# Performance work log

Measured on AMD Instinct MI355X. Metric: run time of the kernel, lower is better.

## Reference

```python
import jax, jax.numpy as jnp
import numpy as np

B, C, L, D, P, Q = 8, 32, 512, 128, 96, 3
LEVELS = 3
ORDERS = [1, 2, 3, 4]  # begin_order=1 + band index

# db4 decomposition low-pass filter (pywt convention)
_LO = np.array([-0.010597401784997278, 0.032883011666982945,
                0.030841381835986965, -0.18703481171888114,
                -0.02798376941698385, 0.6308807679295904,
                0.7148465705525415, 0.23037781330885523], dtype=np.float32)
FLEN = int(_LO.size)
_HI = (_LO[::-1] * ((-1.0) ** (np.arange(FLEN) + 1))).astype(np.float32)

DEC_LO_R = jnp.asarray(_LO[::-1].copy())  # correlation kernel = reversed dec_lo
DEC_HI_R = jnp.asarray(_HI[::-1].copy())
REC_LO_R = jnp.asarray(_LO.copy())        # rec_lo[::-1] == dec_lo (orthogonal wavelet)
REC_HI_R = jnp.asarray(_HI.copy())        # rec_hi[::-1] == dec_hi


def _corr(x, k, stride=1, pad=0):
    # batched 1D correlation; x: [N, Lx], k: [flen]
    return jax.lax.conv_general_dilated(
        x[:, None, :], k[None, None, :], (stride,), [(pad, pad)],
        dimension_numbers=('NCH', 'OIH', 'NCH'))[:, 0, :]


def dwt_step(x):
    # pywt.dwt, mode='symmetric': half-sample symmetric extension by flen-1,
    # correlate with reversed filter, sample odd positions. out len = (n+flen-1)//2
    p = FLEN - 1
    ext = jnp.concatenate([x[:, :p][:, ::-1], x, x[:, -p:][:, ::-1]], axis=1)
    e = ext[:, 1:]
    return _corr(e, DEC_LO_R, stride=2), _corr(e, DEC_HI_R, stride=2)


def idwt_step(a, d):
    # pywt.idwt: upsample-by-2, full convolution with rec filters, trim flen-2 per side
    n = a.shape[1]
    z = jnp.zeros((a.shape[0], 2 * n - 1), a.dtype)
    ua = z.at[:, ::2].set(a)
    ud = z.at[:, ::2].set(d)
    y = _corr(ua, REC_LO_R, pad=FLEN - 1) + _corr(ud, REC_HI_R, pad=FLEN - 1)
    t = FLEN - 2
    return y[:, t:y.shape[1] - t]


def dwt_bands(x):
    # x: [N, L] -> LEVELS+1 single-band reconstructions (wavedec + selective waverec)
    n = x.shape[1]
    a, dets = x, []
    for _ in range(LEVELS):
        a, d = dwt_step(a)
        dets.append(d)
    clist = [a] + dets[::-1]  # [cA_L, cD_L, ..., cD_1]
    bands = []
    for i in range(len(clist)):
        keep = [c if j == i else jnp.zeros_like(c) for j, c in enumerate(clist)]
        r = keep[0]
        for d in keep[1:]:
            if r.shape[1] == d.shape[1] + 1:  # pywt waverec length fixup
                r = r[:, :-1]
            r = idwt_step(r, d)
        bands.append(r[:, :n])
    return bands


def embed(x1, w):
    # TokenEmbedding: Conv1d(1, D, k=3, padding=1, circular, bias=False); x_mark=None
    xp = jnp.concatenate([x1[:, -1:], x1, x1[:, :1]], axis=1)[:, None, :]
    y = jax.lax.conv_general_dilated(xp, w, (1,), [(0, 0)],
                                     dimension_numbers=('NCH', 'OIH', 'NCH'))
    return y.transpose(0, 2, 1)  # [N, L, D]


def cheby(x, coeffs):
    # ChebyKANLinear: tanh squash, Chebyshev T_0..T_K-1 recurrence, contract with coeffs
    # x: [M, Din], coeffs: [Din, Dout, K]
    x = jnp.tanh(x)
    K = coeffs.shape[2]
    t_prev = jnp.ones_like(x)
    out = t_prev @ coeffs[:, :, 0]
    if K > 1:
        t = x
        out = out + t @ coeffs[:, :, 1]
        for k in range(2, K):
            t, t_prev = 2.0 * x * t - t_prev, t
            out = out + t @ coeffs[:, :, k]
    return out


def conv_same(x, w, b, dil):
    # x: [N, Ch, L]; Conv1d(C, C, 3, padding=dil, dilation=dil)
    y = jax.lax.conv_general_dilated(x, w, (1,), [(dil, dil)], rhs_dilation=(dil,),
                                     dimension_numbers=('NCH', 'OIH', 'NCH'))
    return y + b[None, :, None]


def tcn(x, w1, b1, w2, b2, dil):
    h = x.transpose(0, 2, 1)
    h = jax.nn.gelu(conv_same(h, w1, b1, dil), approximate=False)
    h = jax.nn.gelu(conv_same(h, w2, b2, dil), approximate=False)
    return h.transpose(0, 2, 1) + x  # residual (dropout is eval-mode identity)


def _forward(x_enc, emb_w, chebs, tcns, proj_w, proj_b, pred_w, pred_b):
    bsz = x_enc.shape[0]
    # use_norm=0 -> Normalize is identity; original detaches before CPU DWT
    x = jax.lax.stop_gradient(x_enc)
    xc = x.transpose(0, 2, 1).reshape(bsz * C, L)  # per-channel series
    bands = dwt_bands(xc)
    fused = jnp.zeros((bsz * C, L, D), x_enc.dtype)
    for i, band in enumerate(bands):
        emb = embed(band, emb_w)  # [B*C, L, D]
        x1 = cheby(emb.reshape(-1, D), chebs[i]).reshape(bsz * C, L, D)
        dil = max(1, 2 ** max(ORDERS[i] - 1, 0))
        fused = fused + x1 + tcn(emb, *tcns[i], dil)
    # predict_layer over time, projection over features
    h = jnp.einsum('nld,pl->npd', fused, pred_w) + pred_b[None, :, None]  # [B*C, P, D]
    out = jnp.einsum('npd,qd->npq', h, proj_w) + proj_b                  # [B*C, P, Q]
    return out.reshape(bsz, C, P, Q)[:, 0]  # channel 0, denorm is identity


def setup_inputs() -> dict:
    key = jax.random.key(0)
    ks = iter(jax.random.split(key, 64))
    inp = {'x_enc': jax.random.normal(next(ks), (B, L, C), jnp.float32)}
    inp['emb_w'] = jax.random.normal(next(ks), (D, 1, 3), jnp.float32) * (2.0 / 3.0) ** 0.5
    std = (2.0 / (D * 3)) ** 0.5
    for i, o in enumerate(ORDERS):
        K = o + 1
        inp[f'cheb{i}'] = jax.random.normal(next(ks), (D, D, K), jnp.float32) * (1.0 / (D * K))
        inp[f'tw1_{i}'] = jax.random.normal(next(ks), (D, D, 3), jnp.float32) * std
        inp[f'tb1_{i}'] = jnp.zeros((D,), jnp.float32)
        inp[f'tw2_{i}'] = jax.random.normal(next(ks), (D, D, 3), jnp.float32) * std
        inp[f'tb2_{i}'] = jnp.zeros((D,), jnp.float32)
    inp['proj_w'] = jax.random.normal(next(ks), (Q, D), jnp.float32) * D ** -0.5
    inp['proj_b'] = jnp.zeros((Q,), jnp.float32)
    inp['pred_w'] = jax.random.normal(next(ks), (P, L), jnp.float32) * L ** -0.5
    inp['pred_b'] = jnp.zeros((P,), jnp.float32)
    return inp


def reference(x_enc, emb_w, cheb0, tw1_0, tb1_0, tw2_0, tb2_0,
              cheb1, tw1_1, tb1_1, tw2_1, tb2_1,
              cheb2, tw1_2, tb1_2, tw2_2, tb2_2,
              cheb3, tw1_3, tb1_3, tw2_3, tb2_3,
              proj_w, proj_b, pred_w, pred_b):
    chebs = [cheb0, cheb1, cheb2, cheb3]
    tcns = [(tw1_0, tb1_0, tw2_0, tb2_0), (tw1_1, tb1_1, tw2_1, tb2_1),
            (tw1_2, tb1_2, tw2_2, tb2_2), (tw1_3, tb1_3, tw2_3, tb2_3)]
    return _forward(x_enc, emb_w, chebs, tcns, proj_w, proj_b, pred_w, pred_b)
```

## Files before the change

kernel.cpp:

```cpp
#include <hip/hip_runtime.h>
#include <math.h>

#define NB 8
#define LL 512
#define DD 128
#define PP 96
#define QQ 3

#define WS_BANDS 0
#define WS_CFR   16384
#define WS_WFR   (WS_CFR + 81920)
#define WS_B0    (WS_WFR + 196608)

typedef __attribute__((ext_vector_type(8))) short short8v;
typedef __attribute__((ext_vector_type(4))) float f32x4;

#define MFMA16(a, b, c) __builtin_amdgcn_mfma_f32_16x16x32_bf16(a, b, c, 0, 0, 0)

__device__ __forceinline__ short f2bf(float f) {
  unsigned u = __builtin_bit_cast(unsigned, f);
  unsigned r = (u + 0x7fffu + ((u >> 16) & 1u)) >> 16;
  return (short)r;
}

__device__ __forceinline__ float fast_tanh(float x) {
  float ax = fabsf(x);
  float e = __expf(-2.0f * ax);
  float r = (1.0f - e) / (1.0f + e);
  return x < 0.0f ? -r : r;
}

__device__ __forceinline__ float fast_gelu(float x) {
  float u = 0.7978845608028654f * x * (1.0f + 0.044715f * x * x);
  return 0.5f * x * (1.0f + fast_tanh(u));
}

constexpr float W_LO[8] = {
  -0.010597401784997278f, 0.032883011666982945f, 0.030841381835986965f,
  -0.18703481171888114f, -0.02798376941698385f, 0.6308807679295904f,
  0.7148465705525415f, 0.23037781330885523f
};

__device__ void dwt_level(const float* xin, int n, float* a, float* d,
                          int tid, int nthr) {
  int outn = (n + 5) / 2 + 1;
  for (int j = tid; j < outn; j += nthr) {
    float sa = 0.f, sd = 0.f;
#pragma unroll
    for (int k = 0; k < 8; ++k) {
      int i = 2 * j + k;
      int idx = (i < 6) ? (5 - i) : ((i < n + 6) ? (i - 6) : (2 * n + 5 - i));
      float v = xin[idx];
      sa += v * W_LO[7 - k];
      sd += v * ((k & 1) ? -W_LO[k] : W_LO[k]);
    }
    a[j] = sa;
    d[j] = sd;
  }
}

__device__ void idwt_level(const float* a, const float* d, float* out, int n,
                           int tid, int nthr) {
  int outn = 2 * n - 6;
  for (int t = tid; t < outn; t += nthr) {
    float s = 0.f;
#pragma unroll
    for (int k = 0; k < 8; ++k) {
      int j = t - 1 + k;
      if (j >= 0 && j <= 2 * n - 2 && ((j & 1) == 0)) {
        int m = j >> 1;
        if (a) s += a[m] * W_LO[k];
        if (d) s += d[m] * ((k & 1) ? W_LO[7 - k] : -W_LO[7 - k]);
      }
    }
    out[t] = s;
  }
}

struct PrepArgs {
  const float* x_enc;
  const float* cheb[4];
  const float* w1[4];
  const float* w2[4];
  const float* pred_b;
  const float* proj_w;
  const float* proj_b;
  float* bands;
  short* cfr;
  short* wfr;
  float* b0;
  float* out;
};

__global__ __launch_bounds__(256) void prep_kernel(PrepArgs a) {
  __shared__ float sx[LL];
  __shared__ float a1[259], d1[259], a2[133], d2[133], a3[70], d3[70];
  __shared__ float rA[LL], rB[LL];
  int bid = blockIdx.x, t = threadIdx.x;
  if (bid < 32) {
    int n = bid & 7, band = bid >> 3;
    for (int l = t; l < LL; l += 256)
      sx[l] = a.x_enc[(size_t)n * LL * 32 + (size_t)l * 32];
    __syncthreads();
    dwt_level(sx, 512, a1, d1, t, 256); __syncthreads();
    dwt_level(a1, 259, a2, d2, t, 256); __syncthreads();
    dwt_level(a2, 133, a3, d3, t, 256); __syncthreads();
    idwt_level(band == 0 ? a3 : nullptr, band == 1 ? d3 : nullptr, rA, 70, t, 256);
    __syncthreads();
    idwt_level(rA, band == 2 ? d2 : nullptr, rB, 133, t, 256);
    __syncthreads();
    idwt_level(rB, band == 3 ? d1 : nullptr, rA, 259, t, 256);
    __syncthreads();
    float* dstb = a.bands + ((size_t)band * NB + n) * LL;
    for (int l = t; l < LL; l += 256) dstb[l] = rA[l];
  } else {
    const int CFRG = 20480, WFRG = 49152, B0N = 512, OUTN = NB * PP * QQ;
    const int total = CFRG + WFRG + B0N + OUTN;
    for (int g = (bid - 32) * 256 + t; g < total; g += 128 * 256) {
      if (g < CFRG) {
        int s = g >> 11, r = g & 2047;
        int ks = r >> 9, r2 = r & 511;
        int nt = r2 >> 6, lane = r2 & 63;
        int b = (s >= 6) ? 3 : ((s >= 3) ? 2 : ((s >= 1) ? 1 : 0));
        int off = (b == 3) ? 6 : ((b == 2) ? 3 : ((b == 1) ? 1 : 0));
        int kl = s - off;
        int K = b + 2;
        int din0 = ks * 32 + (lane >> 4) * 8;
        int dout = nt * 16 + (lane & 15);
        const float* src = a.cheb[b];
        short8v v;
#pragma unroll
        for (int el = 0; el < 8; ++el)
          v[el] = f2bf(src[((size_t)(din0 + el) * DD + dout) * K + kl + 1]);
        ((short8v*)a.cfr)[g] = v;
      } else if (g < CFRG + WFRG) {
        int g2 = g - CFRG;
        int m = g2 >> 11, r = g2 & 2047;
        int ks = r >> 9, r2 = r & 511;
        int nt = r2 >> 6, lane = r2 & 63;
        int bw = m / 3, tap = m - bw * 3;
        int band = bw >> 1, which = bw & 1;
        const float* w = which ? a.w2[band] : a.w1[band];
        int din0 = ks * 32 + (lane >> 4) * 8;
        int dout = nt * 16 + (lane & 15);
        short8v v;
#pragma unroll
        for (int el = 0; el < 8; ++el)
          v[el] = f2bf(w[((size_t)dout * DD + din0 + el) * 3 + tap]);
        ((short8v*)a.wfr)[g2] = v;
      } else if (g < CFRG + WFRG + B0N) {
        int e4 = g - CFRG - WFRG;
        int b = e4 >> 7, dout = e4 & 127;
        int K = b + 2;
        const float* cw = a.cheb[b];
        float s2 = 0.f;
        for (int din = 0; din < DD; ++din) s2 += cw[((size_t)din * DD + dout) * K];
        a.b0[e4] = s2;
      } else {
        int e5 = g - CFRG - WFRG - B0N;
        int pq = e5 % (PP * QQ);
        int p = pq / QQ, q = pq - p * QQ;
        float S = 0.f;
        const float* pw = a.proj_w + (size_t)q * DD;
        for (int d = 0; d < DD; ++d) S += pw[d];
        a.out[e5] = a.pred_b[p] * S + a.proj_b[q];
      }
    }
  }
}

struct MainArgs {
  const float* emb_w;
  const float* bands;
  const short* cfr;
  const short* wfr;
  const float* proj_w;
  const float* pred_w;
  const float* b1[4];
  const float* b2[4];
  const float* b0;
  float* out;
};

__device__ __forceinline__ void proj_epilogue(
    const MainArgs& ar, int n, int l0, float* tile, float* red, float* gq) {
  int t = threadIdx.x;
  __syncthreads();
  if (t < 192) {
    int pair = t % 96, half = t / 96;
    int p_loc = pair / 3, q = pair - (pair / 3) * 3;
    const float* pw = ar.proj_w + (size_t)q * DD + half * 64;
    const float* tr = tile + p_loc * 132 + half * 64;
    float sv = 0.f;
#pragma unroll 8
    for (int d = 0; d < 64; ++d) sv += tr[d] * pw[d];
    red[t] = sv;
  }
  __syncthreads();
  if (t < 96) gq[t] = red[t] + red[96 + t];
  __syncthreads();
  if (t < PP) {
    const float* pw = ar.pred_w + (size_t)t * LL + l0;
    float s0 = 0.f, s1 = 0.f, s2 = 0.f;
#pragma unroll 8
    for (int l = 0; l < 32; ++l) {
      float w = pw[l];
      s0 += w * gq[l * 3 + 0];
      s1 += w * gq[l * 3 + 1];
      s2 += w * gq[l * 3 + 2];
    }
    float* op = ar.out + (size_t)n * (PP * QQ) + t * 3;
    atomicAdd(op + 0, s0);
    atomicAdd(op + 1, s1);
    atomicAdd(op + 2, s2);
  }
}

template <int NK>
__device__ __forceinline__ void cheby_core(
    const MainArgs& ar, int band, int n, int l0, short* sU, float* blx,
    float* red, float* gq) {
  int t = threadIdx.x;
  const float* brow = ar.bands + ((size_t)band * NB + n) * LL;
  const float* ew = ar.emb_w;
  if (t < 34) blx[t] = brow[(l0 - 1 + t + LL) & 511];
  __syncthreads();
  for (int idx = t; idx < 32 * DD; idx += 256) {
    int l = idx >> 7, dch = idx & 127;
    float e = ew[dch * 3] * blx[l] + ew[dch * 3 + 1] * blx[l + 1] +
              ew[dch * 3 + 2] * blx[l + 2];
    float x = fast_tanh(e);
    int o = l * 136 + dch;
    sU[o] = f2bf(x);
    if (NK >= 2) {
      float t2 = 2.f * x * x - 1.f;
      sU[4352 + o] = f2bf(t2);
      if (NK >= 3) {
        float t3 = 2.f * x * t2 - x;
        sU[8704 + o] = f2bf(t3);
        if (NK >= 4) sU[13056 + o] = f2bf(2.f * x * t3 - t2);
      }
    }
  }
  __syncthreads();

  int w = t >> 6, lane = t & 63;
  int r16 = lane & 15, kq = lane >> 4;
  const int sbase = NK * (NK - 1) / 2;
  const short8v* cfrv = (const short8v*)ar.cfr;
  f32x4 cacc[2][2];
#pragma unroll
  for (int i = 0; i < 2; ++i)
#pragma unroll
    for (int j = 0; j < 2; ++j) cacc[i][j] = (f32x4){0.f, 0.f, 0.f, 0.f};
#pragma unroll
  for (int s = 0; s < NK; ++s) {
#pragma unroll
    for (int ks = 0; ks < 4; ++ks) {
      short8v a0 = *(const short8v*)&sU[s * 4352 + r16 * 136 + ks * 32 + kq * 8];
      short8v a1 = *(const short8v*)&sU[s * 4352 + (16 + r16) * 136 + ks * 32 + kq * 8];
      short8v bf0 = cfrv[(((sbase + s) * 4 + ks) * 8 + w * 2 + 0) * 64 + lane];
      short8v bf1 = cfrv[(((sbase + s) * 4 + ks) * 8 + w * 2 + 1) * 64 + lane];
      cacc[0][0] = MFMA16(a0, bf0, cacc[0][0]);
      cacc[0][1] = MFMA16(a0, bf1, cacc[0][1]);
      cacc[1][0] = MFMA16(a1, bf0, cacc[1][0]);
      cacc[1][1] = MFMA16(a1, bf1, cacc[1][1]);
    }
  }
  __syncthreads();
  float* tile = (float*)sU;
  int row0 = kq * 4;
#pragma unroll
  for (int nt = 0; nt < 2; ++nt) {
    int dout = w * 32 + nt * 16 + r16;
    float b0v = ar.b0[band * DD + dout];
#pragma unroll
    for (int m = 0; m < 2; ++m)
#pragma unroll
      for (int r = 0; r < 4; ++r)
        tile[(m * 16 + row0 + r) * 132 + dout] = cacc[m][nt][r] + b0v;
  }
  proj_epilogue(ar, n, l0, tile, red, gq);
}

template <int DIL>
__device__ __forceinline__ void conv_core(
    const MainArgs& ar, int band, int n, int l0, short* sU, float* blx2,
    float* red, float* gq) {
  int t = threadIdx.x;
  const float* brow = ar.bands + ((size_t)band * NB + n) * LL;
  const float* ew = ar.emb_w;
  if (t < 66) blx2[t] = brow[(l0 - 2 * DIL - 1 + t + LL) & 511];
  __syncthreads();

  const int ETR = 32 + 4 * DIL;
  for (int idx = t; idx < ETR * DD; idx += 256) {
    int v = idx >> 7, dch = idx & 127;
    int l = l0 - 2 * DIL + v;
    float e = 0.f;
    if (l >= 0 && l < LL)
      e = ew[dch * 3] * blx2[v] + ew[dch * 3 + 1] * blx2[v + 1] +
          ew[dch * 3 + 2] * blx2[v + 2];
    sU[v * 136 + dch] = f2bf(e);
  }
  __syncthreads();

  int w = t >> 6, lane = t & 63;
  int r16 = lane & 15, kq = lane >> 4;
  const short8v* wfrv = (const short8v*)ar.wfr;

  const int m3a = (band * 2) * 3;
  f32x4 acc1[3][2];
#pragma unroll
  for (int i = 0; i < 3; ++i)
#pragma unroll
    for (int j = 0; j < 2; ++j) acc1[i][j] = (f32x4){0.f, 0.f, 0.f, 0.f};
#pragma unroll
  for (int tap = 0; tap < 3; ++tap) {
#pragma unroll
    for (int ks = 0; ks < 4; ++ks) {
      short8v bf0 = wfrv[(((m3a + tap) * 4 + ks) * 8 + w * 2 + 0) * 64 + lane];
      short8v bf1 = wfrv[(((m3a + tap) * 4 + ks) * 8 + w * 2 + 1) * 64 + lane];
#pragma unroll
      for (int m = 0; m < 3; ++m) {
        short8v av = *(const short8v*)&sU[(m * 16 + r16 + tap * DIL) * 136 + ks * 32 + kq * 8];
        acc1[m][0] = MFMA16(av, bf0, acc1[m][0]);
        acc1[m][1] = MFMA16(av, bf1, acc1[m][1]);
      }
    }
  }
  {
    float bias0 = ar.b1[band][w * 32 + r16];
    float bias1 = ar.b1[band][w * 32 + 16 + r16];
#pragma unroll
    for (int m = 0; m < 3; ++m)
#pragma unroll
      for (int r = 0; r < 4; ++r) {
        int u = m * 16 + kq * 4 + r;
        int l = l0 - DIL + u;
        bool valid = (l >= 0) && (l < LL) && (u < 32 + 2 * DIL);
        short v0 = valid ? f2bf(fast_gelu(acc1[m][0][r] + bias0)) : (short)0;
        short v1 = valid ? f2bf(fast_gelu(acc1[m][1][r] + bias1)) : (short)0;
        sU[8704 + u * 136 + w * 32 + r16] = v0;
        sU[8704 + u * 136 + w * 32 + 16 + r16] = v1;
      }
  }
  __syncthreads();

  const int m3b = (band * 2 + 1) * 3;
  f32x4 acc2[2][2];
#pragma unroll
  for (int i = 0; i < 2; ++i)
#pragma unroll
    for (int j = 0; j < 2; ++j) acc2[i][j] = (f32x4){0.f, 0.f, 0.f, 0.f};
#pragma unroll
  for (int tap = 0; tap < 3; ++tap) {
#pragma unroll
    for (int ks = 0; ks < 4; ++ks) {
      short8v bf0 = wfrv[(((m3b + tap) * 4 + ks) * 8 + w * 2 + 0) * 64 + lane];
      short8v bf1 = wfrv[(((m3b + tap) * 4 + ks) * 8 + w * 2 + 1) * 64 + lane];
#pragma unroll
      for (int m = 0; m < 2; ++m) {
        short8v av = *(const short8v*)&sU[8704 + (m * 16 + r16 + tap * DIL) * 136 + ks * 32 + kq * 8];
        acc2[m][0] = MFMA16(av, bf0, acc2[m][0]);
        acc2[m][1] = MFMA16(av, bf1, acc2[m][1]);
      }
    }
  }

  float* tile = (float*)sU;
#pragma unroll
  for (int nt = 0; nt < 2; ++nt) {
    int dout = w * 32 + nt * 16 + r16;
    float b2v = ar.b2[band][dout];
    float w0 = ew[dout * 3], w1 = ew[dout * 3 + 1], w2 = ew[dout * 3 + 2];
#pragma unroll
    for (int m = 0; m < 2; ++m)
#pragma unroll
      for (int r = 0; r < 4; ++r) {
        int p = m * 16 + kq * 4 + r;
        float eres = w0 * blx2[p + 2 * DIL] + w1 * blx2[p + 2 * DIL + 1] +
                     w2 * blx2[p + 2 * DIL + 2];
        tile[p * 132 + dout] = fast_gelu(acc2[m][nt][r] + b2v) + eres;
      }
  }
  proj_epilogue(ar, n, l0, tile, red, gq);
}

__global__ __launch_bounds__(256) void main_kernel(MainArgs ar) {
  __shared__ __align__(16) short sU[17408];
  __shared__ float blx[80];
  __shared__ float red[192];
  __shared__ float gq[96];
  int bid = blockIdx.x;
  int role = bid & 1, band = (bid >> 1) & 3, n = (bid >> 3) & 7;
  int l0 = (bid >> 6) << 5;
  if (role == 0) {
    switch (band) {
      case 0: cheby_core<1>(ar, band, n, l0, sU, blx, red, gq); break;
      case 1: cheby_core<2>(ar, band, n, l0, sU, blx, red, gq); break;
      case 2: cheby_core<3>(ar, band, n, l0, sU, blx, red, gq); break;
      default: cheby_core<4>(ar, band, n, l0, sU, blx, red, gq); break;
    }
  } else {
    switch (band) {
      case 0: conv_core<1>(ar, band, n, l0, sU, blx, red, gq); break;
      case 1: conv_core<2>(ar, band, n, l0, sU, blx, red, gq); break;
      case 2: conv_core<4>(ar, band, n, l0, sU, blx, red, gq); break;
      default: conv_core<8>(ar, band, n, l0, sU, blx, red, gq); break;
    }
  }
}

extern "C" void kernel_launch(void* const* d_in, const int* in_sizes, int n_in,
                              void* d_out, int out_size, void* d_ws, size_t ws_size,
                              hipStream_t stream) {
  const float* emb_w = (const float*)d_in[1];
  const float* proj_w = (const float*)d_in[22];
  const float* proj_b = (const float*)d_in[23];
  const float* pred_w = (const float*)d_in[24];
  const float* pred_b = (const float*)d_in[25];
  float* ws = (float*)d_ws;
  float* bands = ws + WS_BANDS;
  short* cfr = (short*)(ws + WS_CFR);
  short* wfr = (short*)(ws + WS_WFR);
  float* b0 = ws + WS_B0;
  float* out = (float*)d_out;

  PrepArgs pa;
  pa.x_enc = (const float*)d_in[0];
  for (int i = 0; i < 4; ++i) {
    pa.cheb[i] = (const float*)d_in[2 + 5 * i];
    pa.w1[i] = (const float*)d_in[3 + 5 * i];
    pa.w2[i] = (const float*)d_in[5 + 5 * i];
  }
  pa.pred_b = pred_b; pa.proj_w = proj_w; pa.proj_b = proj_b;
  pa.bands = bands; pa.cfr = cfr; pa.wfr = wfr; pa.b0 = b0; pa.out = out;

  MainArgs ma;
  ma.emb_w = emb_w; ma.bands = bands; ma.cfr = cfr; ma.wfr = wfr;
  ma.proj_w = proj_w; ma.pred_w = pred_w;
  for (int i = 0; i < 4; ++i) {
    ma.b1[i] = (const float*)d_in[4 + 5 * i];
    ma.b2[i] = (const float*)d_in[6 + 5 * i];
  }
  ma.b0 = b0; ma.out = out;

  prep_kernel<<<160, 256, 0, stream>>>(pa);
  main_kernel<<<1024, 256, 0, stream>>>(ma);
}
```

Before: 36.32 us.

## Halve main kernel LDS by two-phase Chebyshev staging and reusing conv buffer

The Chebyshev path now stages only T1/T2 in shared memory, runs their MFMAs, then recomputes tanh and writes T3/T4 into the same buffer for a second MFMA pass. The conv path writes the intermediate GELU tile over the input region instead of a separate offset, with extra barriers added. Together these cut the shared array from 17408 to 8704 shorts, aiming for more resident blocks per CU. The cost is recomputing the embedding and tanh for higher orders and a few added __syncthreads.

```diff
diff --git a/kernel.cpp b/kernel.cpp
--- a/kernel.cpp
+++ b/kernel.cpp
@@ -232,15 +232,7 @@
     float x = fast_tanh(e);
     int o = l * 136 + dch;
     sU[o] = f2bf(x);
-    if (NK >= 2) {
-      float t2 = 2.f * x * x - 1.f;
-      sU[4352 + o] = f2bf(t2);
-      if (NK >= 3) {
-        float t3 = 2.f * x * t2 - x;
-        sU[8704 + o] = f2bf(t3);
-        if (NK >= 4) sU[13056 + o] = f2bf(2.f * x * t3 - t2);
-      }
-    }
+    if (NK >= 2) sU[4352 + o] = f2bf(2.f * x * x - 1.f);
   }
   __syncthreads();
 
@@ -253,8 +245,10 @@
   for (int i = 0; i < 2; ++i)
 #pragma unroll
     for (int j = 0; j < 2; ++j) cacc[i][j] = (f32x4){0.f, 0.f, 0.f, 0.f};
-#pragma unroll
-  for (int s = 0; s < NK; ++s) {
+
+  const int NC1 = (NK >= 2) ? 2 : 1;
+#pragma unroll
+  for (int s = 0; s < NC1; ++s) {
 #pragma unroll
     for (int ks = 0; ks < 4; ++ks) {
       short8v a0 = *(const short8v*)&sU[s * 4352 + r16 * 136 + ks * 32 + kq * 8];
@@ -267,6 +261,34 @@
       cacc[1][1] = MFMA16(a1, bf1, cacc[1][1]);
     }
   }
+  if (NK >= 3) {
+    __syncthreads();
+    for (int idx = t; idx < 32 * DD; idx += 256) {
+      int l = idx >> 7, dch = idx & 127;
+      float e = ew[dch * 3] * blx[l] + ew[dch * 3 + 1] * blx[l + 1] +
+                ew[dch * 3 + 2] * blx[l + 2];
+      float x = fast_tanh(e);
+      float x2 = x * x;
+      int o = l * 136 + dch;
+      sU[o] = f2bf(x * (4.f * x2 - 3.f));
+      if (NK >= 4) sU[4352 + o] = f2bf(8.f * x2 * (x2 - 1.f) + 1.f);
+    }
+    __syncthreads();
+#pragma unroll
+    for (int s = 2; s < NK; ++s) {
+#pragma unroll
+      for (int ks = 0; ks < 4; ++ks) {
+        short8v a0 = *(const short8v*)&sU[(s - 2) * 4352 + r16 * 136 + ks * 32 + kq * 8];
+        short8v a1 = *(const short8v*)&sU[(s - 2) * 4352 + (16 + r16) * 136 + ks * 32 + kq * 8];
+        short8v bf0 = cfrv[(((sbase + s) * 4 + ks) * 8 + w * 2 + 0) * 64 + lane];
+        short8v bf1 = cfrv[(((sbase + s) * 4 + ks) * 8 + w * 2 + 1) * 64 + lane];
+        cacc[0][0] = MFMA16(a0, bf0, cacc[0][0]);
+        cacc[0][1] = MFMA16(a0, bf1, cacc[0][1]);
+        cacc[1][0] = MFMA16(a1, bf0, cacc[1][0]);
+        cacc[1][1] = MFMA16(a1, bf1, cacc[1][1]);
+      }
+    }
+  }
   __syncthreads();
   float* tile = (float*)sU;
   int row0 = kq * 4;
@@ -329,6 +351,7 @@
       }
     }
   }
+  __syncthreads();
   {
     float bias0 = ar.b1[band][w * 32 + r16];
     float bias1 = ar.b1[band][w * 32 + 16 + r16];
@@ -341,8 +364,8 @@
         bool valid = (l >= 0) && (l < LL) && (u < 32 + 2 * DIL);
         short v0 = valid ? f2bf(fast_gelu(acc1[m][0][r] + bias0)) : (short)0;
         short v1 = valid ? f2bf(fast_gelu(acc1[m][1][r] + bias1)) : (short)0;
-        sU[8704 + u * 136 + w * 32 + r16] = v0;
-        sU[8704 + u * 136 + w * 32 + 16 + r16] = v1;
+        sU[u * 136 + w * 32 + r16] = v0;
+        sU[u * 136 + w * 32 + 16 + r16] = v1;
       }
   }
   __syncthreads();
@@ -361,12 +384,13 @@
       short8v bf1 = wfrv[(((m3b + tap) * 4 + ks) * 8 + w * 2 + 1) * 64 + lane];
 #pragma unroll
       for (int m = 0; m < 2; ++m) {
-        short8v av = *(const short8v*)&sU[8704 + (m * 16 + r16 + tap * DIL) * 136 + ks * 32 + kq * 8];
+        short8v av = *(const short8v*)&sU[(m * 16 + r16 + tap * DIL) * 136 + ks * 32 + kq * 8];
         acc2[m][0] = MFMA16(av, bf0, acc2[m][0]);
         acc2[m][1] = MFMA16(av, bf1, acc2[m][1]);
       }
     }
   }
+  __syncthreads();
 
   float* tile = (float*)sU;
 #pragma unroll
@@ -388,7 +412,7 @@
 }
 
 __global__ __launch_bounds__(256) void main_kernel(MainArgs ar) {
-  __shared__ __align__(16) short sU[17408];
+  __shared__ __align__(16) short sU[8704];
   __shared__ float blx[80];
   __shared__ float red[192];
   __shared__ float gq[96];
```

Result: slower. 44.96 us (+23.8%).
